# Kernel optimization log

Hardware: AMD Instinct MI355X
Metric: run time of the kernel (lower is better)

The kernel has to match this reference:

```python
import jax, jax.numpy as jnp
import numpy as np

G, N, C, H, L = 128, 512, 64, 4, 4   # graphs, nodes/graph, channels, heads, layers
NT = G * N                            # 65536 total nodes
PE, IN_DIM, PROT = 16, 64, 128
DEG = 16
E = NT * DEG
EPS = 1e-5


def setup_inputs() -> dict:
    key = jax.random.key(0)
    ks = jax.random.split(key, 48)
    def w(k, shape):
        fan = shape[-2] if len(shape) >= 2 else shape[-1]
        return (jax.random.normal(k, shape, jnp.float32) / np.sqrt(fan)).astype(jnp.float32)
    inp = {}
    inp['x'] = jax.random.normal(ks[0], (NT, IN_DIM), jnp.float32)
    inp['pe'] = jax.random.normal(ks[1], (NT, PE), jnp.float32)
    inp['edge_index'] = jax.random.randint(ks[2], (2, E), 0, NT, dtype=jnp.int32)
    # embedding layers
    inp['node_emb_w'] = w(ks[3], (IN_DIM, C - PE)); inp['node_emb_b'] = jnp.zeros((C - PE,), jnp.float32)
    inp['pe_lin_w'] = w(ks[4], (PE, PE));           inp['pe_lin_b'] = jnp.zeros((PE,), jnp.float32)
    inp['pe_norm_g'] = jnp.ones((PE,), jnp.float32); inp['pe_norm_b'] = jnp.zeros((PE,), jnp.float32)
    # per-layer stacked params [L, ...]
    inp['gin_w1'] = w(ks[5], (L, C, C)); inp['gin_b1'] = jnp.zeros((L, C), jnp.float32)
    inp['gin_w2'] = w(ks[6], (L, C, C)); inp['gin_b2'] = jnp.zeros((L, C), jnp.float32)
    inp['attn_wq'] = w(ks[7], (L, C, C)); inp['attn_bq'] = jnp.zeros((L, C), jnp.float32)
    inp['attn_wk'] = w(ks[8], (L, C, C)); inp['attn_bk'] = jnp.zeros((L, C), jnp.float32)
    inp['attn_wv'] = w(ks[9], (L, C, C)); inp['attn_bv'] = jnp.zeros((L, C), jnp.float32)
    inp['attn_wo'] = w(ks[10], (L, C, C)); inp['attn_bo'] = jnp.zeros((L, C), jnp.float32)
    for i, nm in enumerate(['norm1', 'norm2', 'norm3']):
        inp[nm + '_g'] = jnp.ones((L, C), jnp.float32)
        inp[nm + '_b'] = jnp.zeros((L, C), jnp.float32)
    inp['mlp_w1'] = w(ks[11], (L, C, 2 * C)); inp['mlp_b1'] = jnp.zeros((L, 2 * C), jnp.float32)
    inp['mlp_w2'] = w(ks[12], (L, 2 * C, C)); inp['mlp_b2'] = jnp.zeros((L, C), jnp.float32)
    inp['head_w'] = w(ks[13], (C, PROT)); inp['head_b'] = jnp.zeros((PROT,), jnp.float32)
    return inp


def _bn(x, g, b):
    # BatchNorm1d, training-mode batch statistics (biased variance)
    mu = x.mean(axis=0)
    var = jnp.mean((x - mu) ** 2, axis=0)
    return (x - mu) * jax.lax.rsqrt(var + EPS) * g + b


def _mha(xd, wq, bq, wk, bk, wv, bv, wo, bo):
    # xd: [G, N, C] dense per-graph batch (all graphs equal size -> full mask)
    dh = C // H
    q = (xd @ wq + bq).reshape(G, N, H, dh)
    k = (xd @ wk + bk).reshape(G, N, H, dh)
    v = (xd @ wv + bv).reshape(G, N, H, dh)
    s = jnp.einsum('gqhd,gkhd->ghqk', q, k) * (1.0 / np.sqrt(dh))
    a = jax.nn.softmax(s, axis=-1)
    o = jnp.einsum('ghqk,gkhd->gqhd', a, v).reshape(G, N, C)
    return o @ wo + bo


def reference(x, pe, edge_index, node_emb_w, node_emb_b, pe_lin_w, pe_lin_b,
              pe_norm_g, pe_norm_b, gin_w1, gin_b1, gin_w2, gin_b2,
              attn_wq, attn_bq, attn_wk, attn_bk, attn_wv, attn_bv, attn_wo, attn_bo,
              norm1_g, norm1_b, norm2_g, norm2_b, norm3_g, norm3_b,
              mlp_w1, mlp_b1, mlp_w2, mlp_b2, head_w, head_b):
    src, dst = edge_index[0], edge_index[1]
    pe_n = _bn(pe, pe_norm_g, pe_norm_b)
    h = jnp.concatenate([x @ node_emb_w + node_emb_b, pe_n @ pe_lin_w + pe_lin_b], axis=1)  # [NT, C]
    for l in range(L):
        # local: GINConv (eps=0): nn(x + sum_j x_j) via gather + segment_sum
        agg = jax.ops.segment_sum(h[src], dst, num_segments=NT)
        z = h + agg
        hl = jax.nn.relu(z @ gin_w1[l] + gin_b1[l]) @ gin_w2[l] + gin_b2[l]
        hl = _bn(hl + h, norm1_g[l], norm1_b[l])
        # global: dense multihead self-attention per graph
        ha = _mha(h.reshape(G, N, C), attn_wq[l], attn_bq[l], attn_wk[l], attn_bk[l],
                  attn_wv[l], attn_bv[l], attn_wo[l], attn_bo[l]).reshape(NT, C)
        ha = _bn(ha + h, norm2_g[l], norm2_b[l])
        out = hl + ha
        out = out + (jax.nn.relu(out @ mlp_w1[l] + mlp_b1[l]) @ mlp_w2[l] + mlp_b2[l])
        h = _bn(out, norm3_g[l], norm3_b[l])
    pooled = h.reshape(G, N, C).mean(axis=1)  # global_mean_pool over equal-size graphs
    return pooled @ head_w + head_b
```

## Files before the change

kernel.cpp:

```cpp
#include <hip/hip_runtime.h>

typedef unsigned short ushort;
typedef unsigned int uint;
typedef __attribute__((ext_vector_type(8))) short short8;
typedef __attribute__((ext_vector_type(4))) float floatx4;

#define NTOT   65536
#define CH     64
#define NLAYER 4
#define NEDGE  1048576
#define EPSV   1e-5f

#define OW_EMB 0
#define OB_EMB 3072
#define OW_PE  3120
#define OB_PE  3376
#define OG_PEN 3392
#define OB_PEN 3408
#define OW_G1  3424
#define OB_G1  19808
#define OW_G2  20064
#define OB_G2  36448
#define OW_Q   36704
#define OB_Q   53088
#define OW_K   53344
#define OB_K   69728
#define OW_V   69984
#define OB_V   86368
#define OW_O   86624
#define OB_O   103008
#define ON1G   103264
#define ON1B   103520
#define ON2G   103776
#define ON2B   104032
#define ON3G   104288
#define ON3B   104544
#define OW_M1  104800
#define OB_M1  137568
#define OW_M2  138080
#define OB_M2  170848
#define OW_H   171104
#define OB_H   179296
#define TOTW   179424

__device__ __forceinline__ float bf2f(ushort u){ return __uint_as_float(((uint)u) << 16); }
__device__ __forceinline__ ushort f2bf(float f){
    uint u = __float_as_uint(f);
    uint r = (u + 0x7fffu + ((u >> 16) & 1u)) >> 16;
    return (ushort)r;
}
__device__ __forceinline__ float2 bfp2(uint w){
    return make_float2(__uint_as_float(w << 16), __uint_as_float(w & 0xffff0000u));
}
__device__ __forceinline__ short8 ldf(const ushort* p){ return *(const short8*)p; }
__device__ __forceinline__ floatx4 mfma16(short8 a, short8 b, floatx4 c){
    return __builtin_amdgcn_mfma_f32_16x16x32_bf16(a, b, c, 0, 0, 0);
}

__global__ void detect_k(const uint* __restrict__ x, int* __restrict__ flag){
    int lane = threadIdx.x;
    uint w = x[lane];
    uint e = (w >> 7) & 0xffu;
    int ok = (e >= 100u && e <= 140u) ? 1 : 0;
    unsigned long long m = __ballot(ok);
    if (lane == 0) flag[0] = (__popcll(m) >= 48) ? 1 : 0;
}

struct WPtrs { const void* p[30]; };

__global__ void convall_k(WPtrs ptrs, ushort* __restrict__ dst, const int* __restrict__ flag){
    const int offs[31] = {0,3072,3120,3376,3392,3408,3424,19808,20064,36448,36704,
                          53088,53344,69728,69984,86368,86624,103008,103264,103520,
                          103776,104032,104288,104544,104800,137568,138080,170848,
                          171104,179296,179424};
    const int kdt[30] = {64,0,16,0,0,0, 64,0,64,0, 64,0,64,0,64,0,64,0,
                         0,0,0,0,0,0, 64,0,128,0, 64,0};
    const int ndt[30] = {48,0,16,0,0,0, 64,0,64,0, 64,0,64,0,64,0,64,0,
                         0,0,0,0,0,0, 128,0,64,0, 128,0};
    int i = blockIdx.x * blockDim.x + threadIdx.x;
    if (i >= TOTW) return;
    int s = 0;
    while (s < 29 && i >= offs[s + 1]) ++s;
    int j = i - offs[s];
    int srcj = j;
    int K = kdt[s];
    if (K > 0){
        int N = ndt[s], KN = K * N;
        int l = j / KN, r = j - l * KN;
        int n = r / K, k2 = r - n * K;
        srcj = l * KN + k2 * N + n;
    }
    if (*flag) dst[i] = ((const ushort*)ptrs.p[s])[srcj];
    else       dst[i] = f2bf(((const float*)ptrs.p[s])[srcj]);
}

__global__ void pe_stats_k(const void* __restrict__ peraw, const int* __restrict__ flag,
                           float* __restrict__ stats){
    int bf = *flag;
    int t = threadIdx.x;
    int c = t & 15, rb = t >> 4;
    int row0 = blockIdx.x * 256;
    float s = 0.f, ss = 0.f;
    for (int i = 0; i < 16; ++i){
        int r = row0 + rb + 16 * i;
        size_t idx = (size_t)r * 16 + c;
        float v = bf ? bf2f(((const ushort*)peraw)[idx]) : ((const float*)peraw)[idx];
        s += v; ss += v * v;
    }
    __shared__ float red[256];
    red[t] = s; __syncthreads();
    if (t < 16){ float tot = 0.f; for (int j = 0; j < 16; ++j) tot += red[t + 16 * j]; atomicAdd(&stats[t], tot); }
    __syncthreads();
    red[t] = ss; __syncthreads();
    if (t < 16){ float tot = 0.f; for (int j = 0; j < 16; ++j) tot += red[t + 16 * j]; atomicAdd(&stats[64 + t], tot); }
}

__global__ void fin_k(const float* __restrict__ stats, const ushort* __restrict__ g,
                      const ushort* __restrict__ b, float* __restrict__ fin, int nch){
    int c = threadIdx.x;
    if (c >= nch) return;
    float mu  = stats[c] * (1.f / NTOT);
    float var = stats[64 + c] * (1.f / NTOT) - mu * mu;
    float a = rsqrtf(var + EPSV) * bf2f(g[c]);
    fin[c] = a;
    fin[64 + c] = bf2f(b[c]) - mu * a;
}

__global__ void embed_k(const void* __restrict__ xraw, const void* __restrict__ peraw,
                        const int* __restrict__ flag, const ushort* __restrict__ wsa,
                        const float* __restrict__ finpe, ushort* __restrict__ hout){
    __shared__ __align__(16) ushort xb[64 * 72];
    __shared__ __align__(16) ushort pen[64 * 24];
    __shared__ __align__(16) ushort Wes[48 * 72];
    __shared__ __align__(16) ushort Wps[16 * 24];
    int bf = *flag;
    int t = threadIdx.x;
    int row0 = blockIdx.x * 64;
    if (bf){
        const uint* xsrc = (const uint*)((const ushort*)xraw + (size_t)row0 * 64);
        for (int i = t; i < 2048; i += 256){
            int r = i >> 5, u = i & 31;
            ((uint*)(xb + r * 72))[u] = xsrc[i];
        }
    } else {
        const float4* xsrc = (const float4*)((const float*)xraw + (size_t)row0 * 64);
        for (int i = t; i < 1024; i += 256){
            int r = i >> 4, u = i & 15;
            float4 f = xsrc[i];
            ((uint*)(xb + r * 72))[2 * u]     = (uint)f2bf(f.x) | ((uint)f2bf(f.y) << 16);
            ((uint*)(xb + r * 72))[2 * u + 1] = (uint)f2bf(f.z) | ((uint)f2bf(f.w) << 16);
        }
    }
    for (int i = t; i < 1024; i += 256){
        int r = i >> 4, k = i & 15;
        size_t idx = (size_t)(row0 + r) * 16 + k;
        float v = bf ? bf2f(((const ushort*)peraw)[idx]) : ((const float*)peraw)[idx];
        pen[r * 24 + k] = f2bf(v * finpe[k] + finpe[64 + k]);
    }
    for (int i = t; i < 1536; i += 256){
        int r = i >> 5, u = i & 31;
        ((uint*)(Wes + r * 72))[u] = ((const uint*)(wsa + OW_EMB))[i];
    }
    {
        int r = t >> 4, k = t & 15;
        Wps[r * 24 + k] = wsa[OW_PE + t];
    }
    __syncthreads();
    int w = t >> 6, l = t & 63, m = l & 15, quad = l >> 4;
    const short8 zero8 = {0, 0, 0, 0, 0, 0, 0, 0};
    const floatx4 zf4 = {0.f, 0.f, 0.f, 0.f};
    const ushort* ap = xb + (16 * w + m) * 72 + quad * 8;
    short8 a0 = ldf(ap), a1 = ldf(ap + 32);
    short8 ape = (quad < 2) ? ldf(pen + (16 * w + m) * 24 + quad * 8) : zero8;
    #pragma unroll
    for (int nt = 0; nt < 4; ++nt){
        floatx4 c = zf4;
        float bias;
        if (nt < 3){
            const ushort* bp = Wes + (nt * 16 + m) * 72 + quad * 8;
            c = mfma16(a0, ldf(bp), c);
            c = mfma16(a1, ldf(bp + 32), c);
            bias = bf2f(wsa[OB_EMB + nt * 16 + m]);
        } else {
            short8 bpe = (quad < 2) ? ldf(Wps + m * 24 + quad * 8) : zero8;
            c = mfma16(ape, bpe, c);
            bias = bf2f(wsa[OB_PE + m]);
        }
        #pragma unroll
        for (int r = 0; r < 4; ++r)
            hout[(size_t)(row0 + 16 * w + quad * 4 + r) * 64 + nt * 16 + m] = f2bf(c[r] + bias);
    }
}

__global__ void hist_k(const int* __restrict__ dst, int* __restrict__ cnt){
    int stride = gridDim.x * blockDim.x;
    for (int e = blockIdx.x * blockDim.x + threadIdx.x; e < NEDGE; e += stride)
        atomicAdd(&cnt[dst[e]], 1);
}

__global__ void scan_k(const int* __restrict__ cnt, int* __restrict__ offs, int* __restrict__ cur){
    int t = threadIdx.x;
    int base0 = t * 64;
    int s = 0;
    for (int i = 0; i < 64; ++i) s += cnt[base0 + i];
    __shared__ int pref[1024];
    pref[t] = s; __syncthreads();
    for (int off = 1; off < 1024; off <<= 1){
        int v = (t >= off) ? pref[t - off] : 0;
        __syncthreads();
        pref[t] += v;
        __syncthreads();
    }
    int run = pref[t] - s;
    for (int i = 0; i < 64; ++i){
        offs[base0 + i] = run;
        cur[base0 + i]  = run;
        run += cnt[base0 + i];
    }
    if (t == 1023) offs[65536] = run;
}

__global__ void scatter_k(const int* __restrict__ src, const int* __restrict__ dst,
                          int* __restrict__ cur, int* __restrict__ csr){
    int stride = gridDim.x * blockDim.x;
    for (int e = blockIdx.x * blockDim.x + threadIdx.x; e < NEDGE; e += stride){
        int p = atomicAdd(&cur[dst[e]], 1);
        csr[p] = src[e];
    }
}

__global__ void agg_k(const ushort* __restrict__ h, const int* __restrict__ offs,
                      const int* __restrict__ csr, ushort* __restrict__ z){
    int w = threadIdx.x >> 6, l = threadIdx.x & 63;
    int node = blockIdx.x * 8 + w * 2 + (l >> 5);
    int c2 = l & 31;
    const uint* hp = (const uint*)h;
    int beg = offs[node], end = offs[node + 1];
    float2 s = bfp2(hp[(size_t)node * 32 + c2]);
    for (int i = beg; i < end; ++i){
        int sn = csr[i];
        float2 p = bfp2(hp[(size_t)sn * 32 + c2]);
        s.x += p.x; s.y += p.y;
    }
    ((uint*)z)[(size_t)node * 32 + c2] = (uint)f2bf(s.x) | ((uint)f2bf(s.y) << 16);
}

__global__ void ginqkv_k(const ushort* __restrict__ z, const ushort* __restrict__ h,
                         const ushort* __restrict__ W1, const ushort* __restrict__ b1,
                         const ushort* __restrict__ W2, const ushort* __restrict__ b2,
                         const ushort* __restrict__ Wq, const ushort* __restrict__ bq,
                         const ushort* __restrict__ Wk, const ushort* __restrict__ bk,
                         const ushort* __restrict__ Wv, const ushort* __restrict__ bv,
                         ushort* __restrict__ zout, ushort* __restrict__ qo,
                         ushort* __restrict__ ko, ushort* __restrict__ vo,
                         float* __restrict__ stats){
    __shared__ __align__(16) ushort As[64 * 72];
    __shared__ __align__(16) ushort Hs[64 * 72];
    __shared__ __align__(16) ushort W1s[64 * 72];
    __shared__ __align__(16) ushort W2s[64 * 72];
    __shared__ __align__(16) ushort Wqs[64 * 72];
    __shared__ __align__(16) ushort Wks[64 * 72];
    __shared__ __align__(16) ushort Wvs[64 * 72];
    __shared__ float sb[128];
    int t = threadIdx.x;
    int row0 = blockIdx.x * 64;
    for (int i = t; i < 2048; i += 256){
        int r = i >> 5, u = i & 31;
        ((uint*)(As  + r * 72))[u] = ((const uint*)(z + (size_t)row0 * 64))[i];
        ((uint*)(Hs  + r * 72))[u] = ((const uint*)(h + (size_t)row0 * 64))[i];
        ((uint*)(W1s + r * 72))[u] = ((const uint*)W1)[i];
        ((uint*)(W2s + r * 72))[u] = ((const uint*)W2)[i];
        ((uint*)(Wqs + r * 72))[u] = ((const uint*)Wq)[i];
        ((uint*)(Wks + r * 72))[u] = ((const uint*)Wk)[i];
        ((uint*)(Wvs + r * 72))[u] = ((const uint*)Wv)[i];
    }
    if (t < 128) sb[t] = 0.f;
    __syncthreads();
    int w = t >> 6, l = t & 63, m = l & 15, q4 = l >> 4;
    const ushort* ap = As + (16 * w + m) * 72 + q4 * 8;
    short8 a0 = ldf(ap), a1 = ldf(ap + 32);
    const ushort* hpp = Hs + (16 * w + m) * 72 + q4 * 8;
    short8 h0 = ldf(hpp), h1 = ldf(hpp + 32);
    floatx4 acc[4];
    #pragma unroll
    for (int nt = 0; nt < 4; ++nt){
        const ushort* bp = W1s + (nt * 16 + m) * 72 + q4 * 8;
        floatx4 c = {0.f, 0.f, 0.f, 0.f};
        c = mfma16(a0, ldf(bp), c);
        c = mfma16(a1, ldf(bp + 32), c);
        acc[nt] = c;
    }
    #pragma unroll
    for (int nt = 0; nt < 4; ++nt){
        float bv = bf2f(b1[nt * 16 + m]);
        #pragma unroll
        for (int r = 0; r < 4; ++r)
            As[(16 * w + q4 * 4 + r) * 72 + nt * 16 + m] = f2bf(fmaxf(acc[nt][r] + bv, 0.f));
    }
    const ushort* ap2 = As + (16 * w + m) * 72 + q4 * 8;
    short8 t0 = ldf(ap2), t1 = ldf(ap2 + 32);
    #pragma unroll
    for (int nt = 0; nt < 4; ++nt){
        const ushort* bp = W2s + (nt * 16 + m) * 72 + q4 * 8;
        floatx4 c = {0.f, 0.f, 0.f, 0.f};
        c = mfma16(t0, ldf(bp), c);
        c = mfma16(t1, ldf(bp + 32), c);
        float bv = bf2f(b2[nt * 16 + m]);
        float vs = 0.f, vss = 0.f;
        #pragma unroll
        for (int r = 0; r < 4; ++r){
            int lr = 16 * w + q4 * 4 + r;
            float val = c[r] + bv + bf2f(Hs[lr * 72 + nt * 16 + m]);
            zout[(size_t)(row0 + lr) * 64 + nt * 16 + m] = f2bf(val);
            vs += val; vss += val * val;
        }
        vs  += __shfl_xor(vs, 16, 64);  vs  += __shfl_xor(vs, 32, 64);
        vss += __shfl_xor(vss, 16, 64); vss += __shfl_xor(vss, 32, 64);
        if (q4 == 0){
            atomicAdd(&sb[nt * 16 + m], vs);
            atomicAdd(&sb[64 + nt * 16 + m], vss);
        }
    }
    ushort* outs[3] = {qo, ko, vo};
    const ushort* bias[3] = {bq, bk, bv};
    const ushort* wmats[3] = {Wqs, Wks, Wvs};
    #pragma unroll
    for (int o = 0; o < 3; ++o){
        #pragma unroll
        for (int nt = 0; nt < 4; ++nt){
            const ushort* bp = wmats[o] + (nt * 16 + m) * 72 + q4 * 8;
            floatx4 c = {0.f, 0.f, 0.f, 0.f};
            c = mfma16(h0, ldf(bp), c);
            c = mfma16(h1, ldf(bp + 32), c);
            float bv2 = bf2f(bias[o][nt * 16 + m]);
            #pragma unroll
            for (int r = 0; r < 4; ++r)
                outs[o][(size_t)(row0 + 16 * w + q4 * 4 + r) * 64 + nt * 16 + m] = f2bf(c[r] + bv2);
        }
    }
    __syncthreads();
    if (t < 64){
        atomicAdd(&stats[t], sb[t]);
        atomicAdd(&stats[64 + t], sb[64 + t]);
    }
}

__global__ void attn_k(ushort* __restrict__ q, const ushort* __restrict__ k,
                       const ushort* __restrict__ v){
    __shared__ __align__(16) ushort Ks[512 * 24];
    __shared__ __align__(16) ushort Vt[16 * 536];
    int t = threadIdx.x;
    int g = blockIdx.x >> 2, head = blockIdx.x & 3;
    int base = g * 512;
    for (int i = t; i < 4096; i += 256){
        int n = i >> 3, u = i & 7;
        uint kw = ((const uint*)(k + (size_t)(base + n) * 64 + head * 16))[u];
        uint vw = ((const uint*)(v + (size_t)(base + n) * 64 + head * 16))[u];
        float2 kf = bfp2(kw);
        Ks[n * 24 + 2 * u]     = f2bf(kf.x * 0.25f);
        Ks[n * 24 + 2 * u + 1] = f2bf(kf.y * 0.25f);
        Vt[(2 * u) * 536 + n]     = (ushort)(vw & 0xffffu);
        Vt[(2 * u + 1) * 536 + n] = (ushort)(vw >> 16);
    }
    __syncthreads();
    int w = t >> 6, l = t & 63, m16 = l & 15, quad = l >> 4;
    const short8 zero8 = {0, 0, 0, 0, 0, 0, 0, 0};
    const floatx4 zf4 = {0.f, 0.f, 0.f, 0.f};
    int key1 = ((m16 >> 2) << 3) + (m16 & 3);

    for (int qi = 0; qi < 8; ++qi){
        int qt = w * 8 + qi;
        int qrow = base + qt * 16 + m16;
        short8 qf = zero8;
        if (quad < 2) qf = ldf(q + (size_t)qrow * 64 + head * 16 + quad * 8);
        floatx4 O = zf4;
        float mm = -1e30f, ll = 0.f;
        for (int kg = 0; kg < 16; ++kg){
            int kb = kg * 32;
            short8 af1 = zero8, af2 = zero8;
            if (quad < 2){
                const ushort* kp = Ks + (kb + key1) * 24 + quad * 8;
                af1 = ldf(kp);
                af2 = ldf(kp + 96);
            }
            floatx4 s1 = mfma16(af1, qf, zf4);
            floatx4 s2 = mfma16(af2, qf, zf4);
            float tm = fmaxf(fmaxf(fmaxf(s1[0], s1[1]), fmaxf(s1[2], s1[3])),
                             fmaxf(fmaxf(s2[0], s2[1]), fmaxf(s2[2], s2[3])));
            tm = fmaxf(tm, __shfl_xor(tm, 16, 64));
            tm = fmaxf(tm, __shfl_xor(tm, 32, 64));
            float mn = fmaxf(mm, tm);
            float c = __expf(mm - mn);
            float p0 = __expf(s1[0] - mn), p1 = __expf(s1[1] - mn);
            float p2 = __expf(s1[2] - mn), p3 = __expf(s1[3] - mn);
            float p4 = __expf(s2[0] - mn), p5 = __expf(s2[1] - mn);
            float p6 = __expf(s2[2] - mn), p7 = __expf(s2[3] - mn);
            float ts = ((p0 + p1) + (p2 + p3)) + ((p4 + p5) + (p6 + p7));
            ts += __shfl_xor(ts, 16, 64);
            ts += __shfl_xor(ts, 32, 64);
            ll = ll * c + ts;
            mm = mn;
            short8 pf;
            pf[0] = (short)f2bf(p0); pf[1] = (short)f2bf(p1);
            pf[2] = (short)f2bf(p2); pf[3] = (short)f2bf(p3);
            pf[4] = (short)f2bf(p4); pf[5] = (short)f2bf(p5);
            pf[6] = (short)f2bf(p6); pf[7] = (short)f2bf(p7);
            short8 vf = ldf(Vt + m16 * 536 + kb + quad * 8);
            O[0] *= c; O[1] *= c; O[2] *= c; O[3] *= c;
            O = mfma16(vf, pf, O);
        }
        float inv = 1.f / ll;
        uint lo = (uint)f2bf(O[0] * inv) | ((uint)f2bf(O[1] * inv) << 16);
        uint hi = (uint)f2bf(O[2] * inv) | ((uint)f2bf(O[3] * inv) << 16);
        uint2 st = {lo, hi};
        *(uint2*)(q + (size_t)qrow * 64 + head * 16 + quad * 4) = st;
    }
}

__global__ void oproj_k(ushort* __restrict__ o, const ushort* __restrict__ h,
                        const ushort* __restrict__ Wo, const ushort* __restrict__ bo,
                        float* __restrict__ stats){
    __shared__ __align__(16) ushort As[64 * 72];
    __shared__ __align__(16) ushort Ws[64 * 72];
    __shared__ float sb[128];
    int t = threadIdx.x;
    int row0 = blockIdx.x * 64;
    for (int i = t; i < 2048; i += 256){
        int r = i >> 5, u = i & 31;
        ((uint*)(As + r * 72))[u] = ((const uint*)(o + (size_t)row0 * 64))[i];
        ((uint*)(Ws + r * 72))[u] = ((const uint*)Wo)[i];
    }
    if (t < 128) sb[t] = 0.f;
    __syncthreads();
    int w = t >> 6, l = t & 63, m = l & 15, q4 = l >> 4;
    const ushort* ap = As + (16 * w + m) * 72 + q4 * 8;
    short8 a0 = ldf(ap), a1 = ldf(ap + 32);
    #pragma unroll
    for (int nt = 0; nt < 4; ++nt){
        const ushort* bp = Ws + (nt * 16 + m) * 72 + q4 * 8;
        floatx4 c = {0.f, 0.f, 0.f, 0.f};
        c = mfma16(a0, ldf(bp), c);
        c = mfma16(a1, ldf(bp + 32), c);
        float bv = bf2f(bo[nt * 16 + m]);
        float vs = 0.f, vss = 0.f;
        #pragma unroll
        for (int r = 0; r < 4; ++r){
            size_t gi = (size_t)(row0 + 16 * w + q4 * 4 + r) * 64 + nt * 16 + m;
            float val = c[r] + bv + bf2f(h[gi]);
            o[gi] = f2bf(val);
            vs += val; vss += val * val;
        }
        vs  += __shfl_xor(vs, 16, 64);  vs  += __shfl_xor(vs, 32, 64);
        vss += __shfl_xor(vss, 16, 64); vss += __shfl_xor(vss, 32, 64);
        if (q4 == 0){
            atomicAdd(&sb[nt * 16 + m], vs);
            atomicAdd(&sb[64 + nt * 16 + m], vss);
        }
    }
    __syncthreads();
    if (t < 64){
        atomicAdd(&stats[t], sb[t]);
        atomicAdd(&stats[64 + t], sb[64 + t]);
    }
}

__global__ void comb_k(ushort* __restrict__ hlpre, const ushort* __restrict__ hapre,
                       const float* __restrict__ st1, const ushort* __restrict__ n1g,
                       const ushort* __restrict__ n1b,
                       const float* __restrict__ st2, const ushort* __restrict__ n2g,
                       const ushort* __restrict__ n2b,
                       const ushort* __restrict__ W1, const ushort* __restrict__ b1,
                       const ushort* __restrict__ W2, const ushort* __restrict__ b2,
                       float* __restrict__ stats){
    __shared__ __align__(16) ushort Ob[64 * 72];
    __shared__ float Of[64 * 64];
    __shared__ __align__(16) ushort W1s[128 * 72];
    __shared__ __align__(16) ushort Hs[64 * 136];
    __shared__ __align__(16) ushort W2s[64 * 136];
    __shared__ float sb[128];
    __shared__ float sf1[128], sf2[128];
    int t = threadIdx.x;
    int row0 = blockIdx.x * 64;
    if (t < 128){
        const float* st = (t < 64) ? st1 : st2;
        const ushort* g = (t < 64) ? n1g : n2g;
        const ushort* b = (t < 64) ? n1b : n2b;
        float* f = (t < 64) ? sf1 : sf2;
        int c = t & 63;
        float mu  = st[c] * (1.f / NTOT);
        float var = st[64 + c] * (1.f / NTOT) - mu * mu;
        float a = rsqrtf(var + EPSV) * bf2f(g[c]);
        f[c] = a;
        f[64 + c] = bf2f(b[c]) - mu * a;
        sb[t] = 0.f;
    }
    __syncthreads();
    for (int i = t; i < 2048; i += 256){
        int r = i >> 5, u = i & 31;
        size_t gi = (size_t)(row0 + r) * 32 + u;
        uint wl = ((const uint*)hlpre)[gi], wa = ((const uint*)hapre)[gi];
        int c0 = u * 2;
        float2 pl = bfp2(wl), pa = bfp2(wa);
        float v0 = pl.x * sf1[c0] + sf1[64 + c0] + pa.x * sf2[c0] + sf2[64 + c0];
        float v1 = pl.y * sf1[c0 + 1] + sf1[64 + c0 + 1] + pa.y * sf2[c0 + 1] + sf2[64 + c0 + 1];
        ((uint*)(Ob + r * 72))[u] = (uint)f2bf(v0) | ((uint)f2bf(v1) << 16);
        Of[r * 64 + c0] = v0; Of[r * 64 + c0 + 1] = v1;
    }
    for (int i = t; i < 4096; i += 256){
        int r = i >> 5, u = i & 31;
        ((uint*)(W1s + r * 72))[u] = ((const uint*)W1)[i];
        int r2 = i >> 6, u2 = i & 63;
        ((uint*)(W2s + r2 * 136))[u2] = ((const uint*)W2)[i];
    }
    __syncthreads();
    int w = t >> 6, l = t & 63, m = l & 15, q4 = l >> 4;
    const ushort* ap = Ob + (16 * w + m) * 72 + q4 * 8;
    short8 a0 = ldf(ap), a1 = ldf(ap + 32);
    #pragma unroll
    for (int nt = 0; nt < 8; ++nt){
        const ushort* bp = W1s + (nt * 16 + m) * 72 + q4 * 8;
        floatx4 c = {0.f, 0.f, 0.f, 0.f};
        c = mfma16(a0, ldf(bp), c);
        c = mfma16(a1, ldf(bp + 32), c);
        float bv = bf2f(b1[nt * 16 + m]);
        #pragma unroll
        for (int r = 0; r < 4; ++r)
            Hs[(16 * w + q4 * 4 + r) * 136 + nt * 16 + m] = f2bf(fmaxf(c[r] + bv, 0.f));
    }
    const ushort* ap2 = Hs + (16 * w + m) * 136 + q4 * 8;
    short8 h0 = ldf(ap2), h1 = ldf(ap2 + 32), h2 = ldf(ap2 + 64), h3 = ldf(ap2 + 96);
    #pragma unroll
    for (int nt = 0; nt < 4; ++nt){
        const ushort* bp = W2s + (nt * 16 + m) * 136 + q4 * 8;
        floatx4 c = {0.f, 0.f, 0.f, 0.f};
        c = mfma16(h0, ldf(bp), c);
        c = mfma16(h1, ldf(bp + 32), c);
        c = mfma16(h2, ldf(bp + 64), c);
        c = mfma16(h3, ldf(bp + 96), c);
        float bv = bf2f(b2[nt * 16 + m]);
        float vs = 0.f, vss = 0.f;
        #pragma unroll
        for (int r = 0; r < 4; ++r){
            int lr = 16 * w + q4 * 4 + r;
            float val = c[r] + bv + Of[lr * 64 + nt * 16 + m];
            hlpre[(size_t)(row0 + lr) * 64 + nt * 16 + m] = f2bf(val);
            vs += val; vss += val * val;
        }
        vs  += __shfl_xor(vs, 16, 64);  vs  += __shfl_xor(vs, 32, 64);
        vss += __shfl_xor(vss, 16, 64); vss += __shfl_xor(vss, 32, 64);
        if (q4 == 0){
            atomicAdd(&sb[nt * 16 + m], vs);
            atomicAdd(&sb[64 + nt * 16 + m], vss);
        }
    }
    __syncthreads();
    if (t < 64){
        atomicAdd(&stats[t], sb[t]);
        atomicAdd(&stats[64 + t], sb[64 + t]);
    }
}

__global__ void bnapply_k(const ushort* __restrict__ in, const float* __restrict__ st3,
                          const ushort* __restrict__ g3, const ushort* __restrict__ b3,
                          ushort* __restrict__ out){
    __shared__ float sf[128];
    int t = threadIdx.x;
    if (t < 64){
        float mu  = st3[t] * (1.f / NTOT);
        float var = st3[64 + t] * (1.f / NTOT) - mu * mu;
        float a = rsqrtf(var + EPSV) * bf2f(g3[t]);
        sf[t] = a;
        sf[64 + t] = bf2f(b3[t]) - mu * a;
    }
    __syncthreads();
    int stride = gridDim.x * blockDim.x;
    const uint* in2 = (const uint*)in;
    uint* out2 = (uint*)out;
    for (int i = blockIdx.x * blockDim.x + t; i < NTOT * CH / 2; i += stride){
        uint w = in2[i];
        float2 p = bfp2(w);
        int cu = (i & 31) * 2;
        float a = p.x * sf[cu] + sf[64 + cu];
        float b = p.y * sf[cu + 1] + sf[64 + cu + 1];
        out2[i] = (uint)f2bf(a) | ((uint)f2bf(b) << 16);
    }
}

__global__ void pool_head_k(const ushort* __restrict__ h, const ushort* __restrict__ Wh,
                            const ushort* __restrict__ bh, const int* __restrict__ flag,
                            void* __restrict__ out){
    __shared__ float red[256];
    __shared__ float pooled[64];
    int t = threadIdx.x, g = blockIdx.x;
    int c = t & 63, rb = t >> 6;
    float s = 0.f;
    for (int ii = 0; ii < 128; ++ii){
        int r = rb + 4 * ii;
        s += bf2f(h[(size_t)(g * 512 + r) * 64 + c]);
    }
    red[t] = s; __syncthreads();
    if (t < 64) pooled[t] = (red[t] + red[64 + t] + red[128 + t] + red[192 + t]) * (1.f / 512.f);
    __syncthreads();
    if (t < 128){
        float a = bf2f(bh[t]);
        #pragma unroll
        for (int k = 0; k < 64; ++k) a += pooled[k] * bf2f(Wh[t * 64 + k]);
        if (*flag) ((ushort*)out)[(size_t)g * 128 + t] = f2bf(a);
        else       ((float*)out)[(size_t)g * 128 + t] = a;
    }
}

extern "C" void kernel_launch(void* const* d_in, const int* in_sizes, int n_in,
                              void* d_out, int out_size, void* d_ws, size_t ws_size,
                              hipStream_t stream){
    const void* x  = d_in[0];
    const void* pe = d_in[1];
    const int* eidx = (const int*)d_in[2];

    char* ws = (char*)d_ws;
    const size_t MB = 1024 * 1024;
    const size_t KB = 1024;
    ushort* h_buf = (ushort*)(ws);
    ushort* z_buf = (ushort*)(ws + 8 * MB);
    ushort* q_buf = (ushort*)(ws + 16 * MB);
    ushort* k_buf = (ushort*)(ws + 24 * MB);
    ushort* v_buf = (ushort*)(ws + 32 * MB);
    int* csr   = (int*)(ws + 40 * MB);
    int* offs  = (int*)(ws + 44 * MB);
    int* cnt   = (int*)(ws + 44 * MB + 384 * KB);
    int* cur   = (int*)(ws + 44 * MB + 640 * KB);
    float* stats = (float*)(ws + 44 * MB + 896 * KB);
    float* fin   = (float*)(ws + 44 * MB + 904 * KB);
    int*   flag  = (int*)(ws + 44 * MB + 912 * KB);
    ushort* wsa  = (ushort*)(ws + 45 * MB);

    hipMemsetAsync(stats, 0, 13 * 128 * sizeof(float), stream);
    hipMemsetAsync(cnt, 0, 65536 * sizeof(int), stream);

    detect_k<<<1, 64, 0, stream>>>((const uint*)x, flag);

    WPtrs wp;
    for (int i = 0; i < 30; ++i) wp.p[i] = d_in[3 + i];
    convall_k<<<(TOTW + 255) / 256, 256, 0, stream>>>(wp, wsa, flag);

    pe_stats_k<<<256, 256, 0, stream>>>(pe, flag, stats);
    fin_k<<<1, 64, 0, stream>>>(stats, wsa + OG_PEN, wsa + OB_PEN, fin, 16);
    embed_k<<<1024, 256, 0, stream>>>(x, pe, flag, wsa, fin, h_buf);
    hist_k<<<1024, 256, 0, stream>>>(eidx + NEDGE, cnt);
    scan_k<<<1, 1024, 0, stream>>>(cnt, offs, cur);
    scatter_k<<<1024, 256, 0, stream>>>(eidx, eidx + NEDGE, cur, csr);

    for (int l = 0; l < NLAYER; ++l){
        float* st1 = stats + (1 + 3 * l) * 128;
        float* st2 = stats + (2 + 3 * l) * 128;
        float* st3 = stats + (3 + 3 * l) * 128;

        agg_k<<<8192, 256, 0, stream>>>(h_buf, offs, csr, z_buf);
        ginqkv_k<<<1024, 256, 0, stream>>>(z_buf, h_buf,
                                           wsa + OW_G1 + l * 4096, wsa + OB_G1 + l * 64,
                                           wsa + OW_G2 + l * 4096, wsa + OB_G2 + l * 64,
                                           wsa + OW_Q + l * 4096, wsa + OB_Q + l * 64,
                                           wsa + OW_K + l * 4096, wsa + OB_K + l * 64,
                                           wsa + OW_V + l * 4096, wsa + OB_V + l * 64,
                                           z_buf, q_buf, k_buf, v_buf, st1);
        attn_k<<<512, 256, 0, stream>>>(q_buf, k_buf, v_buf);
        oproj_k<<<1024, 256, 0, stream>>>(q_buf, h_buf, wsa + OW_O + l * 4096,
                                          wsa + OB_O + l * 64, st2);
        comb_k<<<1024, 256, 0, stream>>>(z_buf, q_buf,
                                         st1, wsa + ON1G + l * 64, wsa + ON1B + l * 64,
                                         st2, wsa + ON2G + l * 64, wsa + ON2B + l * 64,
                                         wsa + OW_M1 + l * 8192, wsa + OB_M1 + l * 128,
                                         wsa + OW_M2 + l * 8192, wsa + OB_M2 + l * 64, st3);
        bnapply_k<<<2048, 256, 0, stream>>>(z_buf, st3, wsa + ON3G + l * 64,
                                            wsa + ON3B + l * 64, h_buf);
    }
    pool_head_k<<<128, 256, 0, stream>>>(h_buf, wsa + OW_H, wsa + OB_H, flag, d_out);
}
```

Before: 1.269 ms.

## Fold trailing BatchNorm apply into next layer's consumers and drop bnapply kernel

Removes the standalone bnapply kernel per layer. comb_k now writes the pre-norm output straight into h_buf, and the norm3 affine is applied lazily: inside agg_k (scaled sum plus degree-weighted shift), during the H tile load in ginqkv_k, in the residual read in oproj_k, and on the pooled mean in pool_head_k. This saves one full read/write pass over the activations per layer and one launch, at the cost of recomputing the BN finalisation in every block. The scatter store also becomes atomicExch, which adds atomic traffic to the CSR build.

```diff
diff --git a/kernel.cpp b/kernel.cpp
--- a/kernel.cpp
+++ b/kernel.cpp
@@ -56,6 +56,20 @@
 __device__ __forceinline__ floatx4 mfma16(short8 a, short8 b, floatx4 c){
     return __builtin_amdgcn_mfma_f32_16x16x32_bf16(a, b, c, 0, 0, 0);
 }
+__device__ __forceinline__ void bnfin(float* sf, const float* st, const ushort* g,
+                                      const ushort* b, int ident, int t){
+    if (t < 64){
+        float a, bb;
+        if (ident){ a = 1.f; bb = 0.f; }
+        else {
+            float mu  = st[t] * (1.f / NTOT);
+            float var = st[64 + t] * (1.f / NTOT) - mu * mu;
+            a = rsqrtf(var + EPSV) * bf2f(g[t]);
+            bb = bf2f(b[t]) - mu * a;
+        }
+        sf[t] = a; sf[64 + t] = bb;
+    }
+}
 
 __global__ void detect_k(const uint* __restrict__ x, int* __restrict__ flag){
     int lane = threadIdx.x;
@@ -225,13 +239,19 @@
     int stride = gridDim.x * blockDim.x;
     for (int e = blockIdx.x * blockDim.x + threadIdx.x; e < NEDGE; e += stride){
         int p = atomicAdd(&cur[dst[e]], 1);
-        csr[p] = src[e];
+        atomicExch(&csr[p], src[e]);
     }
 }
 
 __global__ void agg_k(const ushort* __restrict__ h, const int* __restrict__ offs,
-                      const int* __restrict__ csr, ushort* __restrict__ z){
-    int w = threadIdx.x >> 6, l = threadIdx.x & 63;
+                      const int* __restrict__ csr, ushort* __restrict__ z,
+                      const float* __restrict__ st, const ushort* __restrict__ g,
+                      const ushort* __restrict__ b, int ident){
+    __shared__ float sf[128];
+    int t = threadIdx.x;
+    bnfin(sf, st, g, b, ident, t);
+    __syncthreads();
+    int w = t >> 6, l = t & 63;
     int node = blockIdx.x * 8 + w * 2 + (l >> 5);
     int c2 = l & 31;
     const uint* hp = (const uint*)h;
@@ -242,10 +262,16 @@
         float2 p = bfp2(hp[(size_t)sn * 32 + c2]);
         s.x += p.x; s.y += p.y;
     }
-    ((uint*)z)[(size_t)node * 32 + c2] = (uint)f2bf(s.x) | ((uint)f2bf(s.y) << 16);
+    float n = (float)(1 + end - beg);
+    int c0 = c2 * 2;
+    float o0 = sf[c0] * s.x + n * sf[64 + c0];
+    float o1 = sf[c0 + 1] * s.y + n * sf[64 + c0 + 1];
+    ((uint*)z)[(size_t)node * 32 + c2] = (uint)f2bf(o0) | ((uint)f2bf(o1) << 16);
 }
 
 __global__ void ginqkv_k(const ushort* __restrict__ z, const ushort* __restrict__ h,
+                         const float* __restrict__ st3, const ushort* __restrict__ g3,
+                         const ushort* __restrict__ b3, int ident,
                          const ushort* __restrict__ W1, const ushort* __restrict__ b1,
                          const ushort* __restrict__ W2, const ushort* __restrict__ b2,
                          const ushort* __restrict__ Wq, const ushort* __restrict__ bq,
@@ -262,19 +288,26 @@
     __shared__ __align__(16) ushort Wks[64 * 72];
     __shared__ __align__(16) ushort Wvs[64 * 72];
     __shared__ float sb[128];
+    __shared__ float sf[128];
     int t = threadIdx.x;
     int row0 = blockIdx.x * 64;
+    bnfin(sf, st3, g3, b3, ident, t);
+    if (t < 128) sb[t] = 0.f;
+    __syncthreads();
     for (int i = t; i < 2048; i += 256){
         int r = i >> 5, u = i & 31;
         ((uint*)(As  + r * 72))[u] = ((const uint*)(z + (size_t)row0 * 64))[i];
-        ((uint*)(Hs  + r * 72))[u] = ((const uint*)(h + (size_t)row0 * 64))[i];
+        uint hv = ((const uint*)(h + (size_t)row0 * 64))[i];
+        int c0 = u * 2;
+        float2 p = bfp2(hv);
+        ((uint*)(Hs + r * 72))[u] = (uint)f2bf(p.x * sf[c0] + sf[64 + c0])
+                                  | ((uint)f2bf(p.y * sf[c0 + 1] + sf[64 + c0 + 1]) << 16);
         ((uint*)(W1s + r * 72))[u] = ((const uint*)W1)[i];
         ((uint*)(W2s + r * 72))[u] = ((const uint*)W2)[i];
         ((uint*)(Wqs + r * 72))[u] = ((const uint*)Wq)[i];
         ((uint*)(Wks + r * 72))[u] = ((const uint*)Wk)[i];
         ((uint*)(Wvs + r * 72))[u] = ((const uint*)Wv)[i];
     }
-    if (t < 128) sb[t] = 0.f;
     __syncthreads();
     int w = t >> 6, l = t & 63, m = l & 15, q4 = l >> 4;
     const ushort* ap = As + (16 * w + m) * 72 + q4 * 8;
@@ -418,19 +451,24 @@
 }
 
 __global__ void oproj_k(ushort* __restrict__ o, const ushort* __restrict__ h,
+                        const float* __restrict__ st3, const ushort* __restrict__ g3,
+                        const ushort* __restrict__ b3, int ident,
                         const ushort* __restrict__ Wo, const ushort* __restrict__ bo,
                         float* __restrict__ stats){
     __shared__ __align__(16) ushort As[64 * 72];
     __shared__ __align__(16) ushort Ws[64 * 72];
     __shared__ float sb[128];
+    __shared__ float sf[128];
     int t = threadIdx.x;
     int row0 = blockIdx.x * 64;
+    bnfin(sf, st3, g3, b3, ident, t);
+    if (t < 128) sb[t] = 0.f;
+    __syncthreads();
     for (int i = t; i < 2048; i += 256){
         int r = i >> 5, u = i & 31;
         ((uint*)(As + r * 72))[u] = ((const uint*)(o + (size_t)row0 * 64))[i];
         ((uint*)(Ws + r * 72))[u] = ((const uint*)Wo)[i];
     }
-    if (t < 128) sb[t] = 0.f;
     __syncthreads();
     int w = t >> 6, l = t & 63, m = l & 15, q4 = l >> 4;
     const ushort* ap = As + (16 * w + m) * 72 + q4 * 8;
@@ -441,20 +479,22 @@
         floatx4 c = {0.f, 0.f, 0.f, 0.f};
         c = mfma16(a0, ldf(bp), c);
         c = mfma16(a1, ldf(bp + 32), c);
-        float bv = bf2f(bo[nt * 16 + m]);
+        int ch = nt * 16 + m;
+        float bv = bf2f(bo[ch]);
+        float ba = sf[ch], bb = sf[64 + ch];
         float vs = 0.f, vss = 0.f;
         #pragma unroll
         for (int r = 0; r < 4; ++r){
-            size_t gi = (size_t)(row0 + 16 * w + q4 * 4 + r) * 64 + nt * 16 + m;
-            float val = c[r] + bv + bf2f(h[gi]);
+            size_t gi = (size_t)(row0 + 16 * w + q4 * 4 + r) * 64 + ch;
+            float val = c[r] + bv + ba * bf2f(h[gi]) + bb;
             o[gi] = f2bf(val);
             vs += val; vss += val * val;
         }
         vs  += __shfl_xor(vs, 16, 64);  vs  += __shfl_xor(vs, 32, 64);
         vss += __shfl_xor(vss, 16, 64); vss += __shfl_xor(vss, 32, 64);
         if (q4 == 0){
-            atomicAdd(&sb[nt * 16 + m], vs);
-            atomicAdd(&sb[64 + nt * 16 + m], vss);
+            atomicAdd(&sb[ch], vs);
+            atomicAdd(&sb[64 + ch], vss);
         }
     }
     __syncthreads();
@@ -464,14 +504,14 @@
     }
 }
 
-__global__ void comb_k(ushort* __restrict__ hlpre, const ushort* __restrict__ hapre,
+__global__ void comb_k(const ushort* __restrict__ hlpre, const ushort* __restrict__ hapre,
                        const float* __restrict__ st1, const ushort* __restrict__ n1g,
                        const ushort* __restrict__ n1b,
                        const float* __restrict__ st2, const ushort* __restrict__ n2g,
                        const ushort* __restrict__ n2b,
                        const ushort* __restrict__ W1, const ushort* __restrict__ b1,
                        const ushort* __restrict__ W2, const ushort* __restrict__ b2,
-                       float* __restrict__ stats){
+                       ushort* __restrict__ hout, float* __restrict__ stats){
     __shared__ __align__(16) ushort Ob[64 * 72];
     __shared__ float Of[64 * 64];
     __shared__ __align__(16) ushort W1s[128 * 72];
@@ -543,7 +583,7 @@
         for (int r = 0; r < 4; ++r){
             int lr = 16 * w + q4 * 4 + r;
             float val = c[r] + bv + Of[lr * 64 + nt * 16 + m];
-            hlpre[(size_t)(row0 + lr) * 64 + nt * 16 + m] = f2bf(val);
+            hout[(size_t)(row0 + lr) * 64 + nt * 16 + m] = f2bf(val);
             vs += val; vss += val * val;
         }
         vs  += __shfl_xor(vs, 16, 64);  vs  += __shfl_xor(vs, 32, 64);
@@ -560,38 +600,15 @@
     }
 }
 
-__global__ void bnapply_k(const ushort* __restrict__ in, const float* __restrict__ st3,
-                          const ushort* __restrict__ g3, const ushort* __restrict__ b3,
-                          ushort* __restrict__ out){
-    __shared__ float sf[128];
-    int t = threadIdx.x;
-    if (t < 64){
-        float mu  = st3[t] * (1.f / NTOT);
-        float var = st3[64 + t] * (1.f / NTOT) - mu * mu;
-        float a = rsqrtf(var + EPSV) * bf2f(g3[t]);
-        sf[t] = a;
-        sf[64 + t] = bf2f(b3[t]) - mu * a;
-    }
-    __syncthreads();
-    int stride = gridDim.x * blockDim.x;
-    const uint* in2 = (const uint*)in;
-    uint* out2 = (uint*)out;
-    for (int i = blockIdx.x * blockDim.x + t; i < NTOT * CH / 2; i += stride){
-        uint w = in2[i];
-        float2 p = bfp2(w);
-        int cu = (i & 31) * 2;
-        float a = p.x * sf[cu] + sf[64 + cu];
-        float b = p.y * sf[cu + 1] + sf[64 + cu + 1];
-        out2[i] = (uint)f2bf(a) | ((uint)f2bf(b) << 16);
-    }
-}
-
-__global__ void pool_head_k(const ushort* __restrict__ h, const ushort* __restrict__ Wh,
-                            const ushort* __restrict__ bh, const int* __restrict__ flag,
-                            void* __restrict__ out){
+__global__ void pool_head_k(const ushort* __restrict__ h, const float* __restrict__ st3,
+                            const ushort* __restrict__ g3, const ushort* __restrict__ b3,
+                            const ushort* __restrict__ Wh, const ushort* __restrict__ bh,
+                            const int* __restrict__ flag, void* __restrict__ out){
     __shared__ float red[256];
     __shared__ float pooled[64];
+    __shared__ float sf[128];
     int t = threadIdx.x, g = blockIdx.x;
+    bnfin(sf, st3, g3, b3, 0, t);
     int c = t & 63, rb = t >> 6;
     float s = 0.f;
     for (int ii = 0; ii < 128; ++ii){
@@ -599,7 +616,9 @@
         s += bf2f(h[(size_t)(g * 512 + r) * 64 + c]);
     }
     red[t] = s; __syncthreads();
-    if (t < 64) pooled[t] = (red[t] + red[64 + t] + red[128 + t] + red[192 + t]) * (1.f / 512.f);
+    if (t < 64)
+        pooled[t] = sf[t] * ((red[t] + red[64 + t] + red[128 + t] + red[192 + t]) * (1.f / 512.f))
+                  + sf[64 + t];
     __syncthreads();
     if (t < 128){
         float a = bf2f(bh[t]);
@@ -654,9 +673,13 @@
         float* st1 = stats + (1 + 3 * l) * 128;
         float* st2 = stats + (2 + 3 * l) * 128;
         float* st3 = stats + (3 + 3 * l) * 128;
-
-        agg_k<<<8192, 256, 0, stream>>>(h_buf, offs, csr, z_buf);
-        ginqkv_k<<<1024, 256, 0, stream>>>(z_buf, h_buf,
+        int ident = (l == 0) ? 1 : 0;
+        const float* stp = (l == 0) ? stats : stats + (3 * l) * 128;
+        const ushort* gp = wsa + ON3G + (l ? (l - 1) : 0) * 64;
+        const ushort* bp = wsa + ON3B + (l ? (l - 1) : 0) * 64;
+
+        agg_k<<<8192, 256, 0, stream>>>(h_buf, offs, csr, z_buf, stp, gp, bp, ident);
+        ginqkv_k<<<1024, 256, 0, stream>>>(z_buf, h_buf, stp, gp, bp, ident,
                                            wsa + OW_G1 + l * 4096, wsa + OB_G1 + l * 64,
                                            wsa + OW_G2 + l * 4096, wsa + OB_G2 + l * 64,
                                            wsa + OW_Q + l * 4096, wsa + OB_Q + l * 64,
@@ -664,15 +687,16 @@
                                            wsa + OW_V + l * 4096, wsa + OB_V + l * 64,
                                            z_buf, q_buf, k_buf, v_buf, st1);
         attn_k<<<512, 256, 0, stream>>>(q_buf, k_buf, v_buf);
-        oproj_k<<<1024, 256, 0, stream>>>(q_buf, h_buf, wsa + OW_O + l * 4096,
-                                          wsa + OB_O + l * 64, st2);
+        oproj_k<<<1024, 256, 0, stream>>>(q_buf, h_buf, stp, gp, bp, ident,
+                                          wsa + OW_O + l * 4096, wsa + OB_O + l * 64, st2);
         comb_k<<<1024, 256, 0, stream>>>(z_buf, q_buf,
                                          st1, wsa + ON1G + l * 64, wsa + ON1B + l * 64,
                                          st2, wsa + ON2G + l * 64, wsa + ON2B + l * 64,
                                          wsa + OW_M1 + l * 8192, wsa + OB_M1 + l * 128,
-                                         wsa + OW_M2 + l * 8192, wsa + OB_M2 + l * 64, st3);
-        bnapply_k<<<2048, 256, 0, stream>>>(z_buf, st3, wsa + ON3G + l * 64,
-                                            wsa + ON3B + l * 64, h_buf);
-    }
-    pool_head_k<<<128, 256, 0, stream>>>(h_buf, wsa + OW_H, wsa + OB_H, flag, d_out);
-}
+                                         wsa + OW_M2 + l * 8192, wsa + OB_M2 + l * 64,
+                                         h_buf, st3);
+    }
+    pool_head_k<<<128, 256, 0, stream>>>(h_buf, stats + 12 * 128,
+                                         wsa + ON3G + 3 * 64, wsa + ON3B + 3 * 64,
+                                         wsa + OW_H, wsa + OB_H, flag, d_out);
+}
```

Result: no change. 1.249 ms (-1.6%).
